# Performance work log

Measured on AMD Instinct MI355X. Metric: run time of the kernel, lower is better.

Reference implementation:

```python
import jax, jax.numpy as jnp
import numpy as np


def _iou(a, b):
    # a: [A,4] boxes, b: [M,4] boxes -> [A,M] IoU (matches torch calc_iou)
    area_a = (a[:, 2] - a[:, 0]) * (a[:, 3] - a[:, 1])
    area_b = (b[:, 2] - b[:, 0]) * (b[:, 3] - b[:, 1])
    iw = jnp.clip(jnp.minimum(a[:, None, 2], b[None, :, 2]) - jnp.maximum(a[:, None, 0], b[None, :, 0]), 0.0)
    ih = jnp.clip(jnp.minimum(a[:, None, 3], b[None, :, 3]) - jnp.maximum(a[:, None, 1], b[None, :, 1]), 0.0)
    inter = iw * ih
    ua = jnp.clip(area_a[:, None] + area_b[None, :] - inter, 1e-8, None)
    return inter / ua


def _boxes(k, shape):
    xy = jax.random.uniform(k, shape + (2,), minval=0.0, maxval=800.0)
    wh = jax.random.uniform(jax.random.fold_in(k, 1), shape + (2,), minval=16.0, maxval=128.0)
    return jnp.concatenate([xy, xy + wh], axis=-1)


def setup_inputs() -> dict:
    B, K, A, C, G = 8, 16, 120000, 2, 32
    key = jax.random.key(0)
    ks = jax.random.split(key, 9)
    anchors = _boxes(ks[0], (1, A))
    patch_img = _boxes(ks[1], (B * K,))
    ann_boxes = _boxes(ks[2], (B, G))
    ann_cls = jax.random.randint(ks[3], (B, G, 1), 0, C).astype(jnp.float32)
    annotations = jnp.concatenate([ann_boxes, ann_cls], axis=-1)  # all valid (col0 != -1)
    classifications = jax.random.uniform(ks[4], (B, A, C), minval=0.02, maxval=0.98)
    regressions = jax.random.normal(ks[5], (B, A, 4)) * 0.1
    patch_score = jax.random.uniform(ks[6], (B * K, 2))
    bbox_id = jax.random.randint(ks[7], (B, K), 0, A)
    label = jax.random.randint(ks[8], (B * K, 1), 0, 2)
    return dict(patch_score=patch_score, classifications=classifications, bbox_id=bbox_id,
                batch_num=B, regressions=regressions, anchors=anchors,
                annotations=annotations, label=label, patch_img=patch_img)


def reference(patch_score, classifications, bbox_id, batch_num, regressions, anchors, annotations, label, patch_img):
    B, A, C = classifications.shape
    K = bbox_id.shape[1]
    N = B * K
    anchor = anchors[0]                                     # [A,4]
    cls_all = jnp.clip(classifications, 1e-5, 1.0 - 1e-5)   # [B,A,C]

    j_idx = jnp.repeat(jnp.arange(B), K)                    # [N] image index per patch
    idx = bbox_id.reshape(-1)                               # [N] anchor id per patch
    is_zero = (label[:, 0] == 0)                            # [N]
    ps0, ps1 = patch_score[:, 0], patch_score[:, 1]

    # --- main suppression term, one per patch (vector over C classes) ---
    cls_sel = cls_all[j_idx, idx]                           # [N,C]
    sup_main = jnp.where(
        is_zero[:, None],
        jnp.maximum(ps1[:, None] - (1.0 - cls_sel) + 0.05, 0.0) - 0.5 * jnp.log(1.0 - cls_sel),
        jnp.maximum(ps0[:, None] - cls_sel + 0.05, 0.0))

    # --- high-IoU neighbour anchors (xx_id): IoU(anchor, patch box) >= 0.6, excluding own anchor ---
    iou_p = _iou(anchor, patch_img).T                       # [N,A]
    mask = (iou_p >= 0.6) & (jnp.arange(A)[None, :] != idx[:, None])  # [N,A]
    cls_b = cls_all[j_idx]                                  # [N,A,C]
    sup_xx = jnp.where(
        is_zero[:, None, None],
        jnp.maximum(ps1[:, None, None] - (1.0 - cls_b) + 0.05, 0.0) - jnp.log(1.0 - cls_b),
        jnp.maximum(ps0[:, None, None] - cls_b + 0.05, 0.0))
    maskf = mask.astype(cls_b.dtype)
    loss_sum = sup_main.sum() + jnp.einsum('nac,na->', sup_xx, maskf)
    rank_count = (N + mask.sum()).astype(loss_sum.dtype)    # len(loss): one element per appended term
    rank_loss = loss_sum / rank_count

    aw = anchor[:, 2] - anchor[:, 0]
    ah = anchor[:, 3] - anchor[:, 1]
    acx = anchor[:, 0] + 0.5 * aw
    acy = anchor[:, 1] + 0.5 * ah
    lab_pos = (label[:, 0] == 1).reshape(B, K).astype(jnp.int32)
    norm = jnp.array([0.1, 0.1, 0.2, 0.2], dtype=regressions.dtype)

    def reg_loss_one(ids_j, pos_j, ann_j, reg_j):
        pos = jnp.zeros(A, jnp.int32).at[ids_j].max(pos_j) > 0  # positive_indices
        iou = _iou(anchor, ann_j[:, :4])                        # [A,G]
        ass = ann_j[jnp.argmax(iou, axis=1)]                    # assigned annotations [A,5]
        gw = ass[:, 2] - ass[:, 0]
        gh = ass[:, 3] - ass[:, 1]
        gcx = ass[:, 0] + 0.5 * gw
        gcy = ass[:, 1] + 0.5 * gh
        gw = jnp.maximum(gw, 1.0)
        gh = jnp.maximum(gh, 1.0)
        t = jnp.stack([(gcx - acx) / aw, (gcy - acy) / ah,
                       jnp.log(gw / aw), jnp.log(gh / ah)], axis=1) / norm
        d = jnp.abs(t - reg_j)                                  # [A,4]
        sl = jnp.where(d <= 1.0 / 9.0, 0.5 * 9.0 * d * d, d - 0.5 / 9.0)
        npos = pos.sum()
        posf = pos.astype(sl.dtype)
        mean_pos = (sl * posf[:, None]).sum() / (jnp.maximum(npos, 1).astype(sl.dtype) * 4.0)
        return jnp.where(npos > 0, mean_pos, 0.0)

    reg_losses = jax.vmap(reg_loss_one)(bbox_id, lab_pos, annotations, regressions)  # [B]
    reg_mean = jnp.mean(reg_losses, keepdims=True)  # [1]
    return rank_loss, reg_mean
```

## Files before the change

kernel.cpp:

```cpp
#include <hip/hip_runtime.h>
#include <hip/hip_bf16.h>


#define A_N 120000
#define B_N 8
#define K_N 16
#define N_N 128
#define G_N 32

__global__ __launch_bounds__(256) void rank_sweep(
    const float* __restrict__ patch_score,
    const float* __restrict__ cls,
    const int* __restrict__ bbox_id,
    const float* __restrict__ anchors,
    const int* __restrict__ label,
    const float* __restrict__ patch_img,
    float* __restrict__ ws_sum,
    unsigned int* __restrict__ ws_cnt)
{
    __shared__ float4 s_box[N_N];
    __shared__ float  s_ab[N_N];
    __shared__ float4 s_meta[N_N];
    int t = threadIdx.x;
    if (t < N_N) {
        float4 b = ((const float4*)patch_img)[t];
        s_box[t] = b;
        s_ab[t]  = (b.z - b.x) * (b.w - b.y);
        int idx = bbox_id[t];
        int lz  = (label[t] == 0) ? 1 : 0;
        float4 m;
        m.x = patch_score[2 * t];
        m.y = patch_score[2 * t + 1];
        m.z = 0.0f;
        m.w = __int_as_float(idx | (lz << 30));
        s_meta[t] = m;
    }
    __syncthreads();

    int a = blockIdx.x * blockDim.x + t;
    float lsum = 0.0f;
    unsigned int lcnt = 0;
    if (a < A_N) {
        float4 ab = ((const float4*)anchors)[a];
        float area_a = (ab.z - ab.x) * (ab.w - ab.y);
        #pragma unroll 4
        for (int n = 0; n < N_N; ++n) {
            float4 bb = s_box[n];
            float iw = fminf(ab.z, bb.z) - fmaxf(ab.x, bb.x);
            float ih = fminf(ab.w, bb.w) - fmaxf(ab.y, bb.y);
            iw = fmaxf(iw, 0.0f);
            ih = fmaxf(ih, 0.0f);
            float inter = iw * ih;
            float ua = fmaxf(area_a + s_ab[n] - inter, 1e-8f);
            if (inter >= 0.6f * ua) {
                float4 mm = s_meta[n];
                int bits = __float_as_int(mm.w);
                int idx  = bits & 0x0fffffff;
                if (a != idx) {
                    lcnt++;
                    int j = n >> 4;
                    const float* cp = cls + ((size_t)j * A_N + a) * 2;
                    float c0 = fminf(fmaxf(cp[0], 1e-5f), 1.0f - 1e-5f);
                    float c1 = fminf(fmaxf(cp[1], 1e-5f), 1.0f - 1e-5f);
                    float contrib;
                    if (bits & (1 << 30)) {
                        contrib = fmaxf(mm.y - (1.0f - c0) + 0.05f, 0.0f) - logf(1.0f - c0)
                                + fmaxf(mm.y - (1.0f - c1) + 0.05f, 0.0f) - logf(1.0f - c1);
                    } else {
                        contrib = fmaxf(mm.x - c0 + 0.05f, 0.0f)
                                + fmaxf(mm.x - c1 + 0.05f, 0.0f);
                    }
                    lsum += contrib;
                }
            }
        }
    }
    for (int off = 32; off > 0; off >>= 1) {
        lsum += __shfl_down(lsum, off, 64);
        lcnt += __shfl_down(lcnt, off, 64);
    }
    __shared__ float s_ps[4];
    __shared__ unsigned int s_pc[4];
    int wave = t >> 6;
    if ((t & 63) == 0) { s_ps[wave] = lsum; s_pc[wave] = lcnt; }
    __syncthreads();
    if (t == 0) {
        float s = s_ps[0] + s_ps[1] + s_ps[2] + s_ps[3];
        unsigned int c = s_pc[0] + s_pc[1] + s_pc[2] + s_pc[3];
        atomicAdd(ws_sum, s);
        atomicAdd(ws_cnt, c);
    }
}

__global__ __launch_bounds__(256) void finalize(
    const float* __restrict__ patch_score,
    const float* __restrict__ cls,
    const int* __restrict__ bbox_id,
    const float* __restrict__ regressions,
    const float* __restrict__ anchors,
    const float* __restrict__ annotations,
    const int* __restrict__ label,
    const float* __restrict__ ws_sum,
    const unsigned int* __restrict__ ws_cnt,
    float* __restrict__ out)
{
    __shared__ float s_ann[B_N * G_N * 5];
    __shared__ int   s_id[N_N];
    __shared__ int   s_lab[N_N];
    __shared__ float s_red[256];
    __shared__ float s_tot[B_N];
    __shared__ int   s_np[B_N];
    int t = threadIdx.x;

    for (int i = t; i < B_N * G_N * 5; i += 256) s_ann[i] = annotations[i];
    if (t < N_N) { s_id[t] = bbox_id[t]; s_lab[t] = label[t]; }
    if (t < B_N) { s_tot[t] = 0.0f; s_np[t] = 0; }
    __syncthreads();

    float v = 0.0f;
    int j = t >> 4;
    int k = t & 15;
    if (t < N_N) {
        int idx = s_id[t];
        bool zero = (s_lab[t] == 0);
        float ps0 = patch_score[2 * t];
        float ps1 = patch_score[2 * t + 1];
        const float* cp = cls + ((size_t)j * A_N + idx) * 2;
        float c0 = fminf(fmaxf(cp[0], 1e-5f), 1.0f - 1e-5f);
        float c1 = fminf(fmaxf(cp[1], 1e-5f), 1.0f - 1e-5f);
        if (zero) {
            v  = fmaxf(ps1 - (1.0f - c0) + 0.05f, 0.0f) - 0.5f * logf(1.0f - c0);
            v += fmaxf(ps1 - (1.0f - c1) + 0.05f, 0.0f) - 0.5f * logf(1.0f - c1);
        } else {
            v  = fmaxf(ps0 - c0 + 0.05f, 0.0f);
            v += fmaxf(ps0 - c1 + 0.05f, 0.0f);
        }
    }
    s_red[t] = v;

    float term = 0.0f;
    int isrep = 0;
    if (t < N_N) {
        int a = s_id[t];
        bool rep = true;
        int posa = 0;
        #pragma unroll
        for (int kk = 0; kk < K_N; ++kk) {
            int aa = s_id[j * K_N + kk];
            if (aa == a) {
                if (kk < k) rep = false;
                if (s_lab[j * K_N + kk] == 1) posa = 1;
            }
        }
        if (rep && posa) {
            isrep = 1;
            float4 ab = ((const float4*)anchors)[a];
            float aw = ab.z - ab.x, ah = ab.w - ab.y;
            float acx = ab.x + 0.5f * aw, acy = ab.y + 0.5f * ah;
            float area_a = aw * ah;
            float best = -1.0f; int bi = 0;
            const float* annj = s_ann + j * G_N * 5;
            #pragma unroll 8
            for (int g = 0; g < G_N; ++g) {
                float bx1 = annj[5 * g + 0], by1 = annj[5 * g + 1];
                float bx2 = annj[5 * g + 2], by2 = annj[5 * g + 3];
                float area_b = (bx2 - bx1) * (by2 - by1);
                float iw = fmaxf(fminf(ab.z, bx2) - fmaxf(ab.x, bx1), 0.0f);
                float ih = fmaxf(fminf(ab.w, by2) - fmaxf(ab.y, by1), 0.0f);
                float inter = iw * ih;
                float ua = fmaxf(area_a + area_b - inter, 1e-8f);
                float iou = inter / ua;
                if (iou > best) { best = iou; bi = g; }
            }
            const float* as_ = annj + 5 * bi;
            float gw = as_[2] - as_[0], gh = as_[3] - as_[1];
            float gcx = as_[0] + 0.5f * gw, gcy = as_[1] + 0.5f * gh;
            gw = fmaxf(gw, 1.0f);
            gh = fmaxf(gh, 1.0f);
            float tt0 = ((gcx - acx) / aw) * 10.0f;
            float tt1 = ((gcy - acy) / ah) * 10.0f;
            float tt2 = logf(gw / aw) * 5.0f;
            float tt3 = logf(gh / ah) * 5.0f;
            float4 rg = ((const float4*)regressions)[(size_t)j * A_N + a];
            float d0 = fabsf(tt0 - rg.x);
            float d1 = fabsf(tt1 - rg.y);
            float d2 = fabsf(tt2 - rg.z);
            float d3 = fabsf(tt3 - rg.w);
            term  = (d0 <= 1.0f / 9.0f) ? 4.5f * d0 * d0 : d0 - 0.5f / 9.0f;
            term += (d1 <= 1.0f / 9.0f) ? 4.5f * d1 * d1 : d1 - 0.5f / 9.0f;
            term += (d2 <= 1.0f / 9.0f) ? 4.5f * d2 * d2 : d2 - 0.5f / 9.0f;
            term += (d3 <= 1.0f / 9.0f) ? 4.5f * d3 * d3 : d3 - 0.5f / 9.0f;
        }
    }
    __syncthreads();
    if (isrep) {
        atomicAdd(&s_tot[j], term);
        atomicAdd(&s_np[j], 1);
    }
    __syncthreads();

    for (int off = 128; off > 0; off >>= 1) {
        if (t < off) s_red[t] += s_red[t + off];
        __syncthreads();
    }

    if (t == 0) {
        float rank = (s_red[0] + ws_sum[0]) / (float)(N_N + ws_cnt[0]);
        out[0] = rank;
        float rs = 0.0f;
        for (int jj = 0; jj < B_N; ++jj)
            rs += (s_np[jj] > 0) ? s_tot[jj] / ((float)s_np[jj] * 4.0f) : 0.0f;
        out[1] = rs / (float)B_N;
    }
}

extern "C" void kernel_launch(void* const* d_in, const int* in_sizes, int n_in,
                              void* d_out, int out_size, void* d_ws, size_t ws_size,
                              hipStream_t stream) {
    const float* patch_score    = (const float*)d_in[0];
    const float* classifications= (const float*)d_in[1];
    const int*   bbox_id        = (const int*)d_in[2];
    const float* regressions    = (const float*)d_in[4];
    const float* anchors        = (const float*)d_in[5];
    const float* annotations    = (const float*)d_in[6];
    const int*   label          = (const int*)d_in[7];
    const float* patch_img      = (const float*)d_in[8];
    float* out = (float*)d_out;

    float* ws_sum = (float*)d_ws;
    unsigned int* ws_cnt = (unsigned int*)((char*)d_ws + sizeof(float));

    hipMemsetAsync(d_ws, 0, 2 * sizeof(float), stream);

    int blocks = (A_N + 255) / 256;
    rank_sweep<<<blocks, 256, 0, stream>>>(patch_score, classifications, bbox_id,
                                           anchors, label, patch_img, ws_sum, ws_cnt);
    finalize<<<1, 256, 0, stream>>>(patch_score, classifications, bbox_id,
                                    regressions, anchors, annotations, label,
                                    ws_sum, ws_cnt, out);
}
```

Measured before the change: 119.4 us.

## Fuse sweep and finalize into one cooperative kernel with grid sync

Merges the anchor sweep and the finalize kernel into a single cooperative launch. One extra block computes the regression loss and the direct patch terms while the sweep blocks run. Per-block partials are written to workspace instead of global atomics, and block 0 reduces them after a grid-wide sync. This removes the memset and a second kernel launch, but adds a grid barrier and the cost of a cooperative launch, which requires all 470 blocks to be resident at once.

Result: slower. 204.6 us (+71.3%).

```diff
diff --git a/kernel.cpp b/kernel.cpp
--- a/kernel.cpp
+++ b/kernel.cpp
@@ -1,5 +1,7 @@
 #include <hip/hip_runtime.h>
-#include <hip/hip_bf16.h>
+#include <hip/hip_cooperative_groups.h>
+
+namespace cg = cooperative_groups;
 
 
 #define A_N 120000
@@ -7,92 +9,10 @@
 #define K_N 16
 #define N_N 128
 #define G_N 32
-
-__global__ __launch_bounds__(256) void rank_sweep(
-    const float* __restrict__ patch_score,
-    const float* __restrict__ cls,
-    const int* __restrict__ bbox_id,
-    const float* __restrict__ anchors,
-    const int* __restrict__ label,
-    const float* __restrict__ patch_img,
-    float* __restrict__ ws_sum,
-    unsigned int* __restrict__ ws_cnt)
-{
-    __shared__ float4 s_box[N_N];
-    __shared__ float  s_ab[N_N];
-    __shared__ float4 s_meta[N_N];
-    int t = threadIdx.x;
-    if (t < N_N) {
-        float4 b = ((const float4*)patch_img)[t];
-        s_box[t] = b;
-        s_ab[t]  = (b.z - b.x) * (b.w - b.y);
-        int idx = bbox_id[t];
-        int lz  = (label[t] == 0) ? 1 : 0;
-        float4 m;
-        m.x = patch_score[2 * t];
-        m.y = patch_score[2 * t + 1];
-        m.z = 0.0f;
-        m.w = __int_as_float(idx | (lz << 30));
-        s_meta[t] = m;
-    }
-    __syncthreads();
-
-    int a = blockIdx.x * blockDim.x + t;
-    float lsum = 0.0f;
-    unsigned int lcnt = 0;
-    if (a < A_N) {
-        float4 ab = ((const float4*)anchors)[a];
-        float area_a = (ab.z - ab.x) * (ab.w - ab.y);
-        #pragma unroll 4
-        for (int n = 0; n < N_N; ++n) {
-            float4 bb = s_box[n];
-            float iw = fminf(ab.z, bb.z) - fmaxf(ab.x, bb.x);
-            float ih = fminf(ab.w, bb.w) - fmaxf(ab.y, bb.y);
-            iw = fmaxf(iw, 0.0f);
-            ih = fmaxf(ih, 0.0f);
-            float inter = iw * ih;
-            float ua = fmaxf(area_a + s_ab[n] - inter, 1e-8f);
-            if (inter >= 0.6f * ua) {
-                float4 mm = s_meta[n];
-                int bits = __float_as_int(mm.w);
-                int idx  = bits & 0x0fffffff;
-                if (a != idx) {
-                    lcnt++;
-                    int j = n >> 4;
-                    const float* cp = cls + ((size_t)j * A_N + a) * 2;
-                    float c0 = fminf(fmaxf(cp[0], 1e-5f), 1.0f - 1e-5f);
-                    float c1 = fminf(fmaxf(cp[1], 1e-5f), 1.0f - 1e-5f);
-                    float contrib;
-                    if (bits & (1 << 30)) {
-                        contrib = fmaxf(mm.y - (1.0f - c0) + 0.05f, 0.0f) - logf(1.0f - c0)
-                                + fmaxf(mm.y - (1.0f - c1) + 0.05f, 0.0f) - logf(1.0f - c1);
-                    } else {
-                        contrib = fmaxf(mm.x - c0 + 0.05f, 0.0f)
-                                + fmaxf(mm.x - c1 + 0.05f, 0.0f);
-                    }
-                    lsum += contrib;
-                }
-            }
-        }
-    }
-    for (int off = 32; off > 0; off >>= 1) {
-        lsum += __shfl_down(lsum, off, 64);
-        lcnt += __shfl_down(lcnt, off, 64);
-    }
-    __shared__ float s_ps[4];
-    __shared__ unsigned int s_pc[4];
-    int wave = t >> 6;
-    if ((t & 63) == 0) { s_ps[wave] = lsum; s_pc[wave] = lcnt; }
-    __syncthreads();
-    if (t == 0) {
-        float s = s_ps[0] + s_ps[1] + s_ps[2] + s_ps[3];
-        unsigned int c = s_pc[0] + s_pc[1] + s_pc[2] + s_pc[3];
-        atomicAdd(ws_sum, s);
-        atomicAdd(ws_cnt, c);
-    }
-}
-
-__global__ __launch_bounds__(256) void finalize(
+#define SWEEP_BLOCKS 469
+#define GRID_BLOCKS (SWEEP_BLOCKS + 1)
+
+__global__ __launch_bounds__(256) void rankloss_all(
     const float* __restrict__ patch_score,
     const float* __restrict__ cls,
     const int* __restrict__ bbox_id,
@@ -100,142 +20,233 @@
     const float* __restrict__ anchors,
     const float* __restrict__ annotations,
     const int* __restrict__ label,
-    const float* __restrict__ ws_sum,
-    const unsigned int* __restrict__ ws_cnt,
+    const float* __restrict__ patch_img,
+    float2* __restrict__ partial,
     float* __restrict__ out)
 {
-    __shared__ float s_ann[B_N * G_N * 5];
-    __shared__ int   s_id[N_N];
-    __shared__ int   s_lab[N_N];
-    __shared__ float s_red[256];
-    __shared__ float s_tot[B_N];
-    __shared__ int   s_np[B_N];
-    int t = threadIdx.x;
-
-    for (int i = t; i < B_N * G_N * 5; i += 256) s_ann[i] = annotations[i];
-    if (t < N_N) { s_id[t] = bbox_id[t]; s_lab[t] = label[t]; }
-    if (t < B_N) { s_tot[t] = 0.0f; s_np[t] = 0; }
-    __syncthreads();
-
-    float v = 0.0f;
-    int j = t >> 4;
-    int k = t & 15;
-    if (t < N_N) {
-        int idx = s_id[t];
-        bool zero = (s_lab[t] == 0);
-        float ps0 = patch_score[2 * t];
-        float ps1 = patch_score[2 * t + 1];
-        const float* cp = cls + ((size_t)j * A_N + idx) * 2;
-        float c0 = fminf(fmaxf(cp[0], 1e-5f), 1.0f - 1e-5f);
-        float c1 = fminf(fmaxf(cp[1], 1e-5f), 1.0f - 1e-5f);
-        if (zero) {
-            v  = fmaxf(ps1 - (1.0f - c0) + 0.05f, 0.0f) - 0.5f * logf(1.0f - c0);
-            v += fmaxf(ps1 - (1.0f - c1) + 0.05f, 0.0f) - 0.5f * logf(1.0f - c1);
-        } else {
-            v  = fmaxf(ps0 - c0 + 0.05f, 0.0f);
-            v += fmaxf(ps0 - c1 + 0.05f, 0.0f);
+    __shared__ float4 s_box[N_N];
+    __shared__ float  s_ab[N_N];
+    __shared__ float4 s_meta[N_N];
+    __shared__ float  s_ann[B_N * G_N * 5];
+    __shared__ float  s_red[256];
+    __shared__ float  s_tot[B_N];
+    __shared__ int    s_np[B_N];
+
+    cg::grid_group grid = cg::this_grid();
+    const int t  = threadIdx.x;
+    const int bx = blockIdx.x;
+
+    if (bx < SWEEP_BLOCKS) {
+        if (t < N_N) {
+            float4 b = ((const float4*)patch_img)[t];
+            s_box[t] = b;
+            s_ab[t]  = (b.z - b.x) * (b.w - b.y);
+            int idx = bbox_id[t];
+            int lz  = (label[t] == 0) ? 1 : 0;
+            float4 m;
+            m.x = patch_score[2 * t];
+            m.y = patch_score[2 * t + 1];
+            m.z = 0.0f;
+            m.w = __int_as_float(idx | (lz << 30));
+            s_meta[t] = m;
+        }
+        __syncthreads();
+
+        int a = bx * 256 + t;
+        float lsum = 0.0f;
+        float lcnt = 0.0f;
+        if (a < A_N) {
+            float4 ab = ((const float4*)anchors)[a];
+            float area_a = (ab.z - ab.x) * (ab.w - ab.y);
+            #pragma unroll 4
+            for (int n = 0; n < N_N; ++n) {
+                float4 bb = s_box[n];
+                float iw = fmaxf(fminf(ab.z, bb.z) - fmaxf(ab.x, bb.x), 0.0f);
+                float ih = fmaxf(fminf(ab.w, bb.w) - fmaxf(ab.y, bb.y), 0.0f);
+                float inter = iw * ih;
+                float ua = fmaxf(area_a + s_ab[n] - inter, 1e-8f);
+                if (inter >= 0.6f * ua) {
+                    float4 mm = s_meta[n];
+                    int bits = __float_as_int(mm.w);
+                    int idx  = bits & 0x0fffffff;
+                    if (a != idx) {
+                        lcnt += 1.0f;
+                        int j = n >> 4;
+                        const float* cp = cls + ((size_t)j * A_N + a) * 2;
+                        float c0 = fminf(fmaxf(cp[0], 1e-5f), 1.0f - 1e-5f);
+                        float c1 = fminf(fmaxf(cp[1], 1e-5f), 1.0f - 1e-5f);
+                        if (bits & (1 << 30)) {
+                            lsum += fmaxf(mm.y - (1.0f - c0) + 0.05f, 0.0f) - logf(1.0f - c0)
+                                  + fmaxf(mm.y - (1.0f - c1) + 0.05f, 0.0f) - logf(1.0f - c1);
+                        } else {
+                            lsum += fmaxf(mm.x - c0 + 0.05f, 0.0f)
+                                  + fmaxf(mm.x - c1 + 0.05f, 0.0f);
+                        }
+                    }
+                }
+            }
+        }
+        for (int off = 32; off > 0; off >>= 1) {
+            lsum += __shfl_down(lsum, off, 64);
+            lcnt += __shfl_down(lcnt, off, 64);
+        }
+        int wave = t >> 6;
+        if ((t & 63) == 0) { s_red[wave] = lsum; s_red[4 + wave] = lcnt; }
+        __syncthreads();
+        if (t == 0) {
+            float2 p;
+            p.x = s_red[0] + s_red[1] + s_red[2] + s_red[3];
+            p.y = s_red[4] + s_red[5] + s_red[6] + s_red[7];
+            partial[bx] = p;
+        }
+    } else {
+        for (int i = t; i < B_N * G_N * 5; i += 256) s_ann[i] = annotations[i];
+        __shared__ int s_id[N_N];
+        __shared__ int s_lab[N_N];
+        if (t < N_N) { s_id[t] = bbox_id[t]; s_lab[t] = label[t]; }
+        if (t < B_N) { s_tot[t] = 0.0f; s_np[t] = 0; }
+        __syncthreads();
+
+        int j = t >> 4;
+        int k = t & 15;
+
+        float v = 0.0f;
+        if (t < N_N) {
+            int idx = s_id[t];
+            bool zero = (s_lab[t] == 0);
+            float ps0 = patch_score[2 * t];
+            float ps1 = patch_score[2 * t + 1];
+            const float* cp = cls + ((size_t)j * A_N + idx) * 2;
+            float c0 = fminf(fmaxf(cp[0], 1e-5f), 1.0f - 1e-5f);
+            float c1 = fminf(fmaxf(cp[1], 1e-5f), 1.0f - 1e-5f);
+            if (zero) {
+                v  = fmaxf(ps1 - (1.0f - c0) + 0.05f, 0.0f) - 0.5f * logf(1.0f - c0);
+                v += fmaxf(ps1 - (1.0f - c1) + 0.05f, 0.0f) - 0.5f * logf(1.0f - c1);
+            } else {
+                v  = fmaxf(ps0 - c0 + 0.05f, 0.0f);
+                v += fmaxf(ps0 - c1 + 0.05f, 0.0f);
+            }
+        }
+        s_red[t] = v;
+
+        float term = 0.0f;
+        int isrep = 0;
+        if (t < N_N) {
+            int a = s_id[t];
+            bool rep = true;
+            int posa = 0;
+            #pragma unroll
+            for (int kk = 0; kk < K_N; ++kk) {
+                int aa = s_id[j * K_N + kk];
+                if (aa == a) {
+                    if (kk < k) rep = false;
+                    if (s_lab[j * K_N + kk] == 1) posa = 1;
+                }
+            }
+            if (rep && posa) {
+                isrep = 1;
+                float4 ab = ((const float4*)anchors)[a];
+                float aw = ab.z - ab.x, ah = ab.w - ab.y;
+                float acx = ab.x + 0.5f * aw, acy = ab.y + 0.5f * ah;
+                float area_a = aw * ah;
+                float best = -1.0f; int bi = 0;
+                const float* annj = s_ann + j * G_N * 5;
+                #pragma unroll 8
+                for (int g = 0; g < G_N; ++g) {
+                    float bx1 = annj[5 * g + 0], by1 = annj[5 * g + 1];
+                    float bx2 = annj[5 * g + 2], by2 = annj[5 * g + 3];
+                    float area_b = (bx2 - bx1) * (by2 - by1);
+                    float iw = fmaxf(fminf(ab.z, bx2) - fmaxf(ab.x, bx1), 0.0f);
+                    float ih = fmaxf(fminf(ab.w, by2) - fmaxf(ab.y, by1), 0.0f);
+                    float inter = iw * ih;
+                    float ua = fmaxf(area_a + area_b - inter, 1e-8f);
+                    float iou = inter / ua;
+                    if (iou > best) { best = iou; bi = g; }
+                }
+                const float* as_ = annj + 5 * bi;
+                float gw = as_[2] - as_[0], gh = as_[3] - as_[1];
+                float gcx = as_[0] + 0.5f * gw, gcy = as_[1] + 0.5f * gh;
+                gw = fmaxf(gw, 1.0f);
+                gh = fmaxf(gh, 1.0f);
+                float tt0 = ((gcx - acx) / aw) * 10.0f;
+                float tt1 = ((gcy - acy) / ah) * 10.0f;
+                float tt2 = logf(gw / aw) * 5.0f;
+                float tt3 = logf(gh / ah) * 5.0f;
+                float4 rg = ((const float4*)regressions)[(size_t)j * A_N + a];
+                float d0 = fabsf(tt0 - rg.x);
+                float d1 = fabsf(tt1 - rg.y);
+                float d2 = fabsf(tt2 - rg.z);
+                float d3 = fabsf(tt3 - rg.w);
+                term  = (d0 <= 1.0f / 9.0f) ? 4.5f * d0 * d0 : d0 - 0.5f / 9.0f;
+                term += (d1 <= 1.0f / 9.0f) ? 4.5f * d1 * d1 : d1 - 0.5f / 9.0f;
+                term += (d2 <= 1.0f / 9.0f) ? 4.5f * d2 * d2 : d2 - 0.5f / 9.0f;
+                term += (d3 <= 1.0f / 9.0f) ? 4.5f * d3 * d3 : d3 - 0.5f / 9.0f;
+            }
+        }
+        __syncthreads();
+        if (isrep) {
+            atomicAdd(&s_tot[j], term);
+            atomicAdd(&s_np[j], 1);
+        }
+        __syncthreads();
+        for (int off = 128; off > 0; off >>= 1) {
+            if (t < off) s_red[t] += s_red[t + off];
+            __syncthreads();
+        }
+        if (t == 0) {
+            partial[SWEEP_BLOCKS] = make_float2(s_red[0], 0.0f);
+            float rs = 0.0f;
+            for (int jj = 0; jj < B_N; ++jj)
+                rs += (s_np[jj] > 0) ? s_tot[jj] / ((float)s_np[jj] * 4.0f) : 0.0f;
+            out[1] = rs / (float)B_N;
         }
     }
-    s_red[t] = v;
-
-    float term = 0.0f;
-    int isrep = 0;
-    if (t < N_N) {
-        int a = s_id[t];
-        bool rep = true;
-        int posa = 0;
-        #pragma unroll
-        for (int kk = 0; kk < K_N; ++kk) {
-            int aa = s_id[j * K_N + kk];
-            if (aa == a) {
-                if (kk < k) rep = false;
-                if (s_lab[j * K_N + kk] == 1) posa = 1;
-            }
-        }
-        if (rep && posa) {
-            isrep = 1;
-            float4 ab = ((const float4*)anchors)[a];
-            float aw = ab.z - ab.x, ah = ab.w - ab.y;
-            float acx = ab.x + 0.5f * aw, acy = ab.y + 0.5f * ah;
-            float area_a = aw * ah;
-            float best = -1.0f; int bi = 0;
-            const float* annj = s_ann + j * G_N * 5;
-            #pragma unroll 8
-            for (int g = 0; g < G_N; ++g) {
-                float bx1 = annj[5 * g + 0], by1 = annj[5 * g + 1];
-                float bx2 = annj[5 * g + 2], by2 = annj[5 * g + 3];
-                float area_b = (bx2 - bx1) * (by2 - by1);
-                float iw = fmaxf(fminf(ab.z, bx2) - fmaxf(ab.x, bx1), 0.0f);
-                float ih = fmaxf(fminf(ab.w, by2) - fmaxf(ab.y, by1), 0.0f);
-                float inter = iw * ih;
-                float ua = fmaxf(area_a + area_b - inter, 1e-8f);
-                float iou = inter / ua;
-                if (iou > best) { best = iou; bi = g; }
-            }
-            const float* as_ = annj + 5 * bi;
-            float gw = as_[2] - as_[0], gh = as_[3] - as_[1];
-            float gcx = as_[0] + 0.5f * gw, gcy = as_[1] + 0.5f * gh;
-            gw = fmaxf(gw, 1.0f);
-            gh = fmaxf(gh, 1.0f);
-            float tt0 = ((gcx - acx) / aw) * 10.0f;
-            float tt1 = ((gcy - acy) / ah) * 10.0f;
-            float tt2 = logf(gw / aw) * 5.0f;
-            float tt3 = logf(gh / ah) * 5.0f;
-            float4 rg = ((const float4*)regressions)[(size_t)j * A_N + a];
-            float d0 = fabsf(tt0 - rg.x);
-            float d1 = fabsf(tt1 - rg.y);
-            float d2 = fabsf(tt2 - rg.z);
-            float d3 = fabsf(tt3 - rg.w);
-            term  = (d0 <= 1.0f / 9.0f) ? 4.5f * d0 * d0 : d0 - 0.5f / 9.0f;
-            term += (d1 <= 1.0f / 9.0f) ? 4.5f * d1 * d1 : d1 - 0.5f / 9.0f;
-            term += (d2 <= 1.0f / 9.0f) ? 4.5f * d2 * d2 : d2 - 0.5f / 9.0f;
-            term += (d3 <= 1.0f / 9.0f) ? 4.5f * d3 * d3 : d3 - 0.5f / 9.0f;
-        }
-    }
-    __syncthreads();
-    if (isrep) {
-        atomicAdd(&s_tot[j], term);
-        atomicAdd(&s_np[j], 1);
-    }
-    __syncthreads();
-
-    for (int off = 128; off > 0; off >>= 1) {
-        if (t < off) s_red[t] += s_red[t + off];
-        __syncthreads();
-    }
-
-    if (t == 0) {
-        float rank = (s_red[0] + ws_sum[0]) / (float)(N_N + ws_cnt[0]);
-        out[0] = rank;
-        float rs = 0.0f;
-        for (int jj = 0; jj < B_N; ++jj)
-            rs += (s_np[jj] > 0) ? s_tot[jj] / ((float)s_np[jj] * 4.0f) : 0.0f;
-        out[1] = rs / (float)B_N;
+
+    __threadfence();
+    grid.sync();
+
+    if (bx == 0) {
+        float s = 0.0f, c = 0.0f;
+        for (int i = t; i < GRID_BLOCKS; i += 256) {
+            float2 p = partial[i];
+            s += p.x;
+            c += p.y;
+        }
+        for (int off = 32; off > 0; off >>= 1) {
+            s += __shfl_down(s, off, 64);
+            c += __shfl_down(c, off, 64);
+        }
+        __syncthreads();
+        int wave = t >> 6;
+        if ((t & 63) == 0) { s_red[wave] = s; s_red[4 + wave] = c; }
+        __syncthreads();
+        if (t == 0) {
+            float sum = s_red[0] + s_red[1] + s_red[2] + s_red[3];
+            float cnt = s_red[4] + s_red[5] + s_red[6] + s_red[7];
+            out[0] = sum / ((float)N_N + cnt);
+        }
     }
 }
 
 extern "C" void kernel_launch(void* const* d_in, const int* in_sizes, int n_in,
                               void* d_out, int out_size, void* d_ws, size_t ws_size,
                               hipStream_t stream) {
-    const float* patch_score    = (const float*)d_in[0];
-    const float* classifications= (const float*)d_in[1];
-    const int*   bbox_id        = (const int*)d_in[2];
-    const float* regressions    = (const float*)d_in[4];
-    const float* anchors        = (const float*)d_in[5];
-    const float* annotations    = (const float*)d_in[6];
-    const int*   label          = (const int*)d_in[7];
-    const float* patch_img      = (const float*)d_in[8];
-    float* out = (float*)d_out;
-
-    float* ws_sum = (float*)d_ws;
-    unsigned int* ws_cnt = (unsigned int*)((char*)d_ws + sizeof(float));
-
-    hipMemsetAsync(d_ws, 0, 2 * sizeof(float), stream);
-
-    int blocks = (A_N + 255) / 256;
-    rank_sweep<<<blocks, 256, 0, stream>>>(patch_score, classifications, bbox_id,
-                                           anchors, label, patch_img, ws_sum, ws_cnt);
-    finalize<<<1, 256, 0, stream>>>(patch_score, classifications, bbox_id,
-                                    regressions, anchors, annotations, label,
-                                    ws_sum, ws_cnt, out);
+    const float* patch_score     = (const float*)d_in[0];
+    const float* classifications = (const float*)d_in[1];
+    const int*   bbox_id         = (const int*)d_in[2];
+    const float* regressions     = (const float*)d_in[4];
+    const float* anchors         = (const float*)d_in[5];
+    const float* annotations     = (const float*)d_in[6];
+    const int*   label           = (const int*)d_in[7];
+    const float* patch_img       = (const float*)d_in[8];
+    float*  out     = (float*)d_out;
+    float2* partial = (float2*)d_ws;
+
+    void* args[] = {
+        (void*)&patch_score, (void*)&classifications, (void*)&bbox_id,
+        (void*)&regressions, (void*)&anchors, (void*)&annotations,
+        (void*)&label, (void*)&patch_img, (void*)&partial, (void*)&out
+    };
+    hipLaunchCooperativeKernel((void*)rankloss_all, dim3(GRID_BLOCKS), dim3(256),
+                               args, 0, stream);
 }
```

## Split patch sweep across two blocks, replace atomics and memset with per-block partials

Applied to the files above, without the earlier changes.

The anchor sweep now splits the 128 patches into two halves handled by separate blocks, doubling the grid. Each block writes a float2 partial (sum, count) instead of doing global atomics, so the memset launch is removed and finalize reduces the partials. The IoU threshold test is rewritten algebraically as inter >= 0.375*(area_a+area_b), which avoids the union computation. The count becomes a float accumulation, and each anchor's classification is now reloaded by two blocks.

After: 103.6 us. 1.15x faster.

```diff
diff --git a/kernel.cpp b/kernel.cpp
--- a/kernel.cpp
+++ b/kernel.cpp
@@ -7,6 +7,10 @@
 #define K_N 16
 #define N_N 128
 #define G_N 32
+#define NSPLIT 2
+#define NH (N_N / NSPLIT)
+#define CHUNKS 469
+#define SWEEP_BLOCKS (CHUNKS * NSPLIT)
 
 __global__ __launch_bounds__(256) void rank_sweep(
     const float* __restrict__ patch_score,
@@ -15,62 +19,56 @@
     const float* __restrict__ anchors,
     const int* __restrict__ label,
     const float* __restrict__ patch_img,
-    float* __restrict__ ws_sum,
-    unsigned int* __restrict__ ws_cnt)
+    float2* __restrict__ partial)
 {
-    __shared__ float4 s_box[N_N];
-    __shared__ float  s_ab[N_N];
-    __shared__ float4 s_meta[N_N];
-    int t = threadIdx.x;
-    if (t < N_N) {
-        float4 b = ((const float4*)patch_img)[t];
+    __shared__ float4 s_box[NH];
+    __shared__ float  s_pab[NH];
+    __shared__ float2 s_ps[NH];
+    __shared__ int    s_bits[NH];
+    __shared__ float  s_w[8];
+    const int t = threadIdx.x;
+    const int chunk = blockIdx.x >> 1;
+    const int nbase = (blockIdx.x & 1) * NH;
+
+    if (t < NH) {
+        int n = nbase + t;
+        float4 b = ((const float4*)patch_img)[n];
         s_box[t] = b;
-        s_ab[t]  = (b.z - b.x) * (b.w - b.y);
-        int idx = bbox_id[t];
-        int lz  = (label[t] == 0) ? 1 : 0;
-        float4 m;
-        m.x = patch_score[2 * t];
-        m.y = patch_score[2 * t + 1];
-        m.z = 0.0f;
-        m.w = __int_as_float(idx | (lz << 30));
-        s_meta[t] = m;
-    }
-    __syncthreads();
-
-    int a = blockIdx.x * blockDim.x + t;
+        s_pab[t] = 0.375f * (b.z - b.x) * (b.w - b.y);
+        s_ps[t]  = ((const float2*)patch_score)[n];
+        s_bits[t] = bbox_id[n] | ((label[n] == 0) ? (1 << 30) : 0);
+    }
+    __syncthreads();
+
+    int a = chunk * 256 + t;
     float lsum = 0.0f;
-    unsigned int lcnt = 0;
+    float lcnt = 0.0f;
     if (a < A_N) {
         float4 ab = ((const float4*)anchors)[a];
-        float area_a = (ab.z - ab.x) * (ab.w - ab.y);
-        #pragma unroll 4
-        for (int n = 0; n < N_N; ++n) {
+        float ca = 0.375f * (ab.z - ab.x) * (ab.w - ab.y);
+        #pragma unroll 8
+        for (int n = 0; n < NH; ++n) {
             float4 bb = s_box[n];
-            float iw = fminf(ab.z, bb.z) - fmaxf(ab.x, bb.x);
-            float ih = fminf(ab.w, bb.w) - fmaxf(ab.y, bb.y);
-            iw = fmaxf(iw, 0.0f);
-            ih = fmaxf(ih, 0.0f);
+            float iw = fmaxf(fminf(ab.z, bb.z) - fmaxf(ab.x, bb.x), 0.0f);
+            float ih = fmaxf(fminf(ab.w, bb.w) - fmaxf(ab.y, bb.y), 0.0f);
             float inter = iw * ih;
-            float ua = fmaxf(area_a + s_ab[n] - inter, 1e-8f);
-            if (inter >= 0.6f * ua) {
-                float4 mm = s_meta[n];
-                int bits = __float_as_int(mm.w);
+            if (inter >= ca + s_pab[n]) {
+                int bits = s_bits[n];
                 int idx  = bits & 0x0fffffff;
                 if (a != idx) {
-                    lcnt++;
-                    int j = n >> 4;
+                    lcnt += 1.0f;
+                    int j = (nbase + n) >> 4;
+                    float2 ps = s_ps[n];
                     const float* cp = cls + ((size_t)j * A_N + a) * 2;
                     float c0 = fminf(fmaxf(cp[0], 1e-5f), 1.0f - 1e-5f);
                     float c1 = fminf(fmaxf(cp[1], 1e-5f), 1.0f - 1e-5f);
-                    float contrib;
                     if (bits & (1 << 30)) {
-                        contrib = fmaxf(mm.y - (1.0f - c0) + 0.05f, 0.0f) - logf(1.0f - c0)
-                                + fmaxf(mm.y - (1.0f - c1) + 0.05f, 0.0f) - logf(1.0f - c1);
+                        lsum += fmaxf(ps.y - (1.0f - c0) + 0.05f, 0.0f) - logf(1.0f - c0)
+                              + fmaxf(ps.y - (1.0f - c1) + 0.05f, 0.0f) - logf(1.0f - c1);
                     } else {
-                        contrib = fmaxf(mm.x - c0 + 0.05f, 0.0f)
-                                + fmaxf(mm.x - c1 + 0.05f, 0.0f);
+                        lsum += fmaxf(ps.x - c0 + 0.05f, 0.0f)
+                              + fmaxf(ps.x - c1 + 0.05f, 0.0f);
                     }
-                    lsum += contrib;
                 }
             }
         }
@@ -79,16 +77,14 @@
         lsum += __shfl_down(lsum, off, 64);
         lcnt += __shfl_down(lcnt, off, 64);
     }
-    __shared__ float s_ps[4];
-    __shared__ unsigned int s_pc[4];
     int wave = t >> 6;
-    if ((t & 63) == 0) { s_ps[wave] = lsum; s_pc[wave] = lcnt; }
+    if ((t & 63) == 0) { s_w[wave] = lsum; s_w[4 + wave] = lcnt; }
     __syncthreads();
     if (t == 0) {
-        float s = s_ps[0] + s_ps[1] + s_ps[2] + s_ps[3];
-        unsigned int c = s_pc[0] + s_pc[1] + s_pc[2] + s_pc[3];
-        atomicAdd(ws_sum, s);
-        atomicAdd(ws_cnt, c);
+        float2 p;
+        p.x = s_w[0] + s_w[1] + s_w[2] + s_w[3];
+        p.y = s_w[4] + s_w[5] + s_w[6] + s_w[7];
+        partial[blockIdx.x] = p;
     }
 }
 
@@ -100,8 +96,7 @@
     const float* __restrict__ anchors,
     const float* __restrict__ annotations,
     const int* __restrict__ label,
-    const float* __restrict__ ws_sum,
-    const unsigned int* __restrict__ ws_cnt,
+    const float2* __restrict__ partial,
     float* __restrict__ out)
 {
     __shared__ float s_ann[B_N * G_N * 5];
@@ -110,30 +105,38 @@
     __shared__ float s_red[256];
     __shared__ float s_tot[B_N];
     __shared__ int   s_np[B_N];
-    int t = threadIdx.x;
+    __shared__ float s_w[8];
+    const int t = threadIdx.x;
+
+    float p_s = 0.0f, p_c = 0.0f;
+    for (int i = t; i < SWEEP_BLOCKS; i += 256) {
+        float2 p = partial[i];
+        p_s += p.x;
+        p_c += p.y;
+    }
 
     for (int i = t; i < B_N * G_N * 5; i += 256) s_ann[i] = annotations[i];
     if (t < N_N) { s_id[t] = bbox_id[t]; s_lab[t] = label[t]; }
     if (t < B_N) { s_tot[t] = 0.0f; s_np[t] = 0; }
     __syncthreads();
 
+    const int j = t >> 4;
+    const int k = t & 15;
+
     float v = 0.0f;
-    int j = t >> 4;
-    int k = t & 15;
     if (t < N_N) {
         int idx = s_id[t];
         bool zero = (s_lab[t] == 0);
-        float ps0 = patch_score[2 * t];
-        float ps1 = patch_score[2 * t + 1];
+        float2 ps = ((const float2*)patch_score)[t];
         const float* cp = cls + ((size_t)j * A_N + idx) * 2;
         float c0 = fminf(fmaxf(cp[0], 1e-5f), 1.0f - 1e-5f);
         float c1 = fminf(fmaxf(cp[1], 1e-5f), 1.0f - 1e-5f);
         if (zero) {
-            v  = fmaxf(ps1 - (1.0f - c0) + 0.05f, 0.0f) - 0.5f * logf(1.0f - c0);
-            v += fmaxf(ps1 - (1.0f - c1) + 0.05f, 0.0f) - 0.5f * logf(1.0f - c1);
+            v  = fmaxf(ps.y - (1.0f - c0) + 0.05f, 0.0f) - 0.5f * logf(1.0f - c0);
+            v += fmaxf(ps.y - (1.0f - c1) + 0.05f, 0.0f) - 0.5f * logf(1.0f - c1);
         } else {
-            v  = fmaxf(ps0 - c0 + 0.05f, 0.0f);
-            v += fmaxf(ps0 - c1 + 0.05f, 0.0f);
+            v  = fmaxf(ps.x - c0 + 0.05f, 0.0f);
+            v += fmaxf(ps.x - c1 + 0.05f, 0.0f);
         }
     }
     s_red[t] = v;
@@ -197,6 +200,13 @@
         atomicAdd(&s_tot[j], term);
         atomicAdd(&s_np[j], 1);
     }
+
+    for (int off = 32; off > 0; off >>= 1) {
+        p_s += __shfl_down(p_s, off, 64);
+        p_c += __shfl_down(p_c, off, 64);
+    }
+    int wave = t >> 6;
+    if ((t & 63) == 0) { s_w[wave] = p_s; s_w[4 + wave] = p_c; }
     __syncthreads();
 
     for (int off = 128; off > 0; off >>= 1) {
@@ -205,8 +215,9 @@
     }
 
     if (t == 0) {
-        float rank = (s_red[0] + ws_sum[0]) / (float)(N_N + ws_cnt[0]);
-        out[0] = rank;
+        float sweep_sum = s_w[0] + s_w[1] + s_w[2] + s_w[3];
+        float sweep_cnt = s_w[4] + s_w[5] + s_w[6] + s_w[7];
+        out[0] = (s_red[0] + sweep_sum) / ((float)N_N + sweep_cnt);
         float rs = 0.0f;
         for (int jj = 0; jj < B_N; ++jj)
             rs += (s_np[jj] > 0) ? s_tot[jj] / ((float)s_np[jj] * 4.0f) : 0.0f;
@@ -217,25 +228,21 @@
 extern "C" void kernel_launch(void* const* d_in, const int* in_sizes, int n_in,
                               void* d_out, int out_size, void* d_ws, size_t ws_size,
                               hipStream_t stream) {
-    const float* patch_score    = (const float*)d_in[0];
-    const float* classifications= (const float*)d_in[1];
-    const int*   bbox_id        = (const int*)d_in[2];
-    const float* regressions    = (const float*)d_in[4];
-    const float* anchors        = (const float*)d_in[5];
-    const float* annotations    = (const float*)d_in[6];
-    const int*   label          = (const int*)d_in[7];
-    const float* patch_img      = (const float*)d_in[8];
-    float* out = (float*)d_out;
-
-    float* ws_sum = (float*)d_ws;
-    unsigned int* ws_cnt = (unsigned int*)((char*)d_ws + sizeof(float));
-
-    hipMemsetAsync(d_ws, 0, 2 * sizeof(float), stream);
-
-    int blocks = (A_N + 255) / 256;
-    rank_sweep<<<blocks, 256, 0, stream>>>(patch_score, classifications, bbox_id,
-                                           anchors, label, patch_img, ws_sum, ws_cnt);
+    const float* patch_score     = (const float*)d_in[0];
+    const float* classifications = (const float*)d_in[1];
+    const int*   bbox_id         = (const int*)d_in[2];
+    const float* regressions     = (const float*)d_in[4];
+    const float* anchors         = (const float*)d_in[5];
+    const float* annotations     = (const float*)d_in[6];
+    const int*   label           = (const int*)d_in[7];
+    const float* patch_img       = (const float*)d_in[8];
+    float*  out     = (float*)d_out;
+    float2* partial = (float2*)d_ws;
+
+    rank_sweep<<<SWEEP_BLOCKS, 256, 0, stream>>>(patch_score, classifications,
+                                                 bbox_id, anchors, label,
+                                                 patch_img, partial);
     finalize<<<1, 256, 0, stream>>>(patch_score, classifications, bbox_id,
                                     regressions, anchors, annotations, label,
-                                    ws_sum, ws_cnt, out);
+                                    partial, out);
 }
```
